# Performance work log

Measured on AMD Instinct MI355X. Metric: run time of the kernel, lower is better.

Reference implementation:

```python
import jax, jax.numpy as jnp
import numpy as np

B, S, D, H = 4, 2048, 1024, 16
DK = D // H
WINDOW = 256
GLOBAL = 16
NEG_INF = float(np.finfo(np.float32).min)


def local_window_mask(seq_len, window, global_tokens):
    # 0 where attention allowed, -inf where |i-j| > window and neither i nor j is a global token
    i = jnp.arange(seq_len)[:, None]
    j = jnp.arange(seq_len)[None, :]
    is_global = (i < global_tokens) | (j < global_tokens)
    out_of_window = jnp.abs(i - j) > window
    return jnp.where(out_of_window & ~is_global, NEG_INF, 0.0).astype(jnp.float32)


def setup_inputs() -> dict:
    key = jax.random.key(0)
    ks = jax.random.split(key, 8)
    std = 1.0 / np.sqrt(D)
    return {
        "q": jax.random.normal(ks[0], (B, S, D), jnp.float32),
        "k": jax.random.normal(ks[1], (B, S, D), jnp.float32),
        "v": jax.random.normal(ks[2], (B, S, D), jnp.float32),
        "attn_mask": jnp.zeros((B, S), jnp.float32),
        "wq": jax.random.normal(ks[3], (D, D), jnp.float32) * std,
        "bq": jnp.zeros((D,), jnp.float32),
        "wk": jax.random.normal(ks[4], (D, D), jnp.float32) * std,
        "bk": jnp.zeros((D,), jnp.float32),
        "wv": jax.random.normal(ks[5], (D, D), jnp.float32) * std,
        "bv": jnp.zeros((D,), jnp.float32),
        "wo": jax.random.normal(ks[6], (D, D), jnp.float32) * std,
        "bo": jnp.zeros((D,), jnp.float32),
    }


def reference(q, k, v, attn_mask, wq, bq, wk, bk, wv, bv, wo, bo):
    b, s, d = q.shape
    # projections (x @ W + b)
    Q = (q @ wq + bq).reshape(b, s, H, DK).transpose(0, 2, 1, 3)  # b h s dk
    K = (k @ wk + bk).reshape(b, s, H, DK).transpose(0, 2, 1, 3)
    V = (v @ wv + bv).reshape(b, s, H, DK).transpose(0, 2, 1, 3)

    scale = 1.0 / np.sqrt(DK)
    scores = jnp.einsum("bhqd,bhkd->bhqk", Q, K) * scale  # b h s s
    # additive key mask broadcast over query positions: attn_mask[:, None, None, :]
    scores = scores + attn_mask[:, None, None, :]
    scores = scores + local_window_mask(s, WINDOW, GLOBAL)[None, None, :, :]
    probs = jax.nn.softmax(scores, axis=-1)
    out = jnp.einsum("bhqk,bhkd->bhqd", probs, V)  # b h s dk
    out = out.transpose(0, 2, 1, 3).reshape(b, s, d)
    return out @ wo + bo
```

## Files before the change

### kernel.cpp

```cpp
#include <hip/hip_runtime.h>


#define B_   4
#define S_   2048
#define D_   1024
#define H_   16
#define DK_  64
#define WIN_ 256
#define GLB_ 16

typedef __attribute__((ext_vector_type(8))) short bf16x8;
typedef __attribute__((ext_vector_type(4))) float floatx4;

__device__ __forceinline__ unsigned short f2bf(float x) {
  unsigned u = __float_as_uint(x);
  unsigned r = u + 0x7FFFu + ((u >> 16) & 1u);
  return (unsigned short)(r >> 16);
}
__device__ __forceinline__ float bf2f(unsigned short h) {
  return __uint_as_float(((unsigned)h) << 16);
}
__device__ __forceinline__ void gload_lds16(const void* g, void* l) {
  __builtin_amdgcn_global_load_lds(
      (const __attribute__((address_space(1))) unsigned int*)g,
      (__attribute__((address_space(3))) unsigned int*)l, 16, 0, 0);
}

__global__ void split_bf16(const float* __restrict__ x,
                           unsigned short* __restrict__ hi,
                           unsigned short* __restrict__ lo)
{
  const int i = blockIdx.x * 256 + threadIdx.x;
  const float4 v = ((const float4*)x)[i];
  unsigned short h0 = f2bf(v.x), h1 = f2bf(v.y), h2 = f2bf(v.z), h3 = f2bf(v.w);
  unsigned short l0 = f2bf(v.x - bf2f(h0)), l1 = f2bf(v.y - bf2f(h1));
  unsigned short l2 = f2bf(v.z - bf2f(h2)), l3 = f2bf(v.w - bf2f(h3));
  unsigned long long hp = (unsigned long long)h0 | ((unsigned long long)h1 << 16)
                        | ((unsigned long long)h2 << 32) | ((unsigned long long)h3 << 48);
  unsigned long long lp = (unsigned long long)l0 | ((unsigned long long)l1 << 16)
                        | ((unsigned long long)l2 << 32) | ((unsigned long long)l3 << 48);
  ((unsigned long long*)hi)[i] = hp;
  ((unsigned long long*)lo)[i] = lp;
}

__global__ void wtsplit(const float* __restrict__ W,
                        unsigned short* __restrict__ hiT,
                        unsigned short* __restrict__ loT)
{
  __shared__ float t[32][33];
  const int bx = blockIdx.x * 32;
  const int by = blockIdx.y * 32;
  const int c = threadIdx.x & 31;
  const int r0 = (threadIdx.x >> 5) * 4;
#pragma unroll
  for (int i = 0; i < 4; ++i)
    t[r0 + i][c] = W[(size_t)(by + r0 + i) * 1024 + bx + c];
  __syncthreads();
#pragma unroll
  for (int i = 0; i < 4; ++i) {
    const int r = r0 + i;
    const float val = t[c][r];
    const unsigned short h = f2bf(val);
    hiT[(size_t)(bx + r) * 1024 + by + c] = h;
    loT[(size_t)(bx + r) * 1024 + by + c] = f2bf(val - bf2f(h));
  }
}

__global__ __launch_bounds__(256, 2) void gemm_mfma(
    const unsigned short* __restrict__ Ahi, const unsigned short* __restrict__ Alo,
    const unsigned short* __restrict__ WThi, const unsigned short* __restrict__ WTlo,
    const float* __restrict__ bias, float* __restrict__ Cf,
    unsigned short* __restrict__ Chi, unsigned short* __restrict__ Clo, int mode)
{
  __shared__ unsigned short AsH[4096], AsL[4096], WsH[4096], WsL[4096];
  const int tid = threadIdx.x;
  const int w = tid >> 6, lane = tid & 63;
  const int wr = w >> 1, wc = w & 1;
  const int bm = blockIdx.y * 128, bn = blockIdx.x * 128;
  const int lrow = lane & 15, lk8 = (lane >> 4) * 8;

  floatx4 acc[4][4];
#pragma unroll
  for (int t = 0; t < 4; ++t)
#pragma unroll
    for (int u = 0; u < 4; ++u) acc[t][u] = (floatx4){0.f, 0.f, 0.f, 0.f};

  const unsigned short* gsrc;
  unsigned short* lbase;
  int growbase;
  if      (w == 0) { gsrc = Ahi;  lbase = AsH; growbase = bm; }
  else if (w == 1) { gsrc = Alo;  lbase = AsL; growbase = bm; }
  else if (w == 2) { gsrc = WThi; lbase = WsH; growbase = bn; }
  else             { gsrc = WTlo; lbase = WsL; growbase = bn; }

  for (int k0 = 0; k0 < 1024; k0 += 32) {
    __syncthreads();
#pragma unroll
    for (int g = 0; g < 8; ++g) {
      const unsigned short* gp =
          gsrc + (size_t)(growbase + g * 16 + lrow) * 1024 + k0 + lk8;
      gload_lds16(gp, lbase + g * 512);
    }
    __syncthreads();

    bf16x8 ah[4], al[4], bh[4], bl[4];
#pragma unroll
    for (int t = 0; t < 4; ++t) {
      ah[t] = *(const bf16x8*)&AsH[(wr * 4 + t) * 512 + lane * 8];
      al[t] = *(const bf16x8*)&AsL[(wr * 4 + t) * 512 + lane * 8];
    }
#pragma unroll
    for (int u = 0; u < 4; ++u) {
      bh[u] = *(const bf16x8*)&WsH[(wc * 4 + u) * 512 + lane * 8];
      bl[u] = *(const bf16x8*)&WsL[(wc * 4 + u) * 512 + lane * 8];
    }
#pragma unroll
    for (int t = 0; t < 4; ++t)
#pragma unroll
      for (int u = 0; u < 4; ++u) {
        acc[t][u] = __builtin_amdgcn_mfma_f32_16x16x32_bf16(al[t], bh[u], acc[t][u], 0, 0, 0);
        acc[t][u] = __builtin_amdgcn_mfma_f32_16x16x32_bf16(ah[t], bl[u], acc[t][u], 0, 0, 0);
        acc[t][u] = __builtin_amdgcn_mfma_f32_16x16x32_bf16(ah[t], bh[u], acc[t][u], 0, 0, 0);
      }
  }

  float bs[4];
#pragma unroll
  for (int u = 0; u < 4; ++u) bs[u] = bias[bn + wc * 64 + u * 16 + lrow];

#pragma unroll
  for (int t = 0; t < 4; ++t)
#pragma unroll
    for (int r = 0; r < 4; ++r) {
      const int row = bm + wr * 64 + t * 16 + (lane >> 4) * 4 + r;
#pragma unroll
      for (int u = 0; u < 4; ++u) {
        const int col = bn + wc * 64 + u * 16 + lrow;
        const float val = acc[t][u][r] + bs[u];
        if (mode == 0) {
          Cf[(size_t)row * 1024 + col] = val;
        } else {
          const int bb = row >> 11, s = row & 2047;
          const int hh = col >> 6, dk = col & 63;
          if (mode == 1) {
            const size_t a = ((size_t)(bb * H_ + hh) * S_ + s) * DK_ + dk;
            const unsigned short hv = f2bf(val);
            Chi[a] = hv;
            Clo[a] = f2bf(val - bf2f(hv));
          } else {
            Chi[((size_t)(bb * H_ + hh) * DK_ + dk) * S_ + s] = f2bf(val);
          }
        }
      }
    }
}

__global__ __launch_bounds__(256, 4) void attn_mfma(
    const unsigned short* __restrict__ Qhi, const unsigned short* __restrict__ Qlo,
    const unsigned short* __restrict__ Khi, const unsigned short* __restrict__ Klo,
    const unsigned short* __restrict__ Vt,  const float* __restrict__ amask,
    unsigned short* __restrict__ AOhi, unsigned short* __restrict__ AOlo)
{
  __shared__ unsigned short lds[16384];

  const int tid = threadIdx.x;
  const int w = tid >> 6, lane = tid & 63;
  const int quad = lane >> 4, lm = lane & 15;
  const int qt = blockIdx.x, h = blockIdx.y, b = blockIdx.z;
  const int i0 = qt * 64;

  const size_t hb = (size_t)(b * H_ + h) * S_ * DK_;
  const unsigned short* Qhih = Qhi + hb;
  const unsigned short* Qloh = Qlo + hb;
  const unsigned short* Khih = Khi + hb;
  const unsigned short* Kloh = Klo + hb;
  const unsigned short* Vth  = Vt  + hb;

  bf16x8 aqh[2], aql[2];
#pragma unroll
  for (int p = 0; p < 2; ++p) {
    const size_t qa = (size_t)(i0 + w * 16 + lm) * DK_ + p * 32 + quad * 8;
    aqh[p] = *(const bf16x8*)(Qhih + qa);
    aql[p] = *(const bf16x8*)(Qloh + qa);
  }

  floatx4 acc_o[4];
  float m_i[4], l_i[4];
#pragma unroll
  for (int u = 0; u < 4; ++u) acc_o[u] = (floatx4){0.f, 0.f, 0.f, 0.f};
#pragma unroll
  for (int r = 0; r < 4; ++r) { m_i[r] = -1e30f; l_i[r] = 0.f; }

  int start, t_lo, t_hi;
  if (qt == 0) { start = 0; t_lo = 0; t_hi = 31; }
  else {
    start = -1;
    t_lo = qt - 4 < 1 ? 1 : qt - 4;
    t_hi = qt + 4 > 31 ? 31 : qt + 4;
  }

  unsigned short* Pb = &lds[12288 + w * 1024];

  for (int tt = start; tt <= t_hi; ++tt) {
    if (tt >= 0 && tt < t_lo) continue;
    const int kt = (tt < 0) ? 0 : tt;
    const int k0 = kt * 64;

    __syncthreads();
    for (int e = w; e < 24; e += 4) {
      const int op = e >> 3, cc = e & 7, g = cc >> 1, hf = cc & 1;
      unsigned short* ldst = &lds[op * 4096 + g * 1024 + hf * 512];
      const unsigned short* gp;
      if (op == 0)      gp = Khih + (size_t)(k0 + g * 16 + lm) * DK_ + (hf * 4 + quad) * 8;
      else if (op == 1) gp = Kloh + (size_t)(k0 + g * 16 + lm) * DK_ + (hf * 4 + quad) * 8;
      else              gp = Vth + (size_t)(g * 16 + lm) * S_ + k0 + (hf * 4 + quad) * 8;
      gload_lds16(gp, ldst);
    }
    __syncthreads();

    floatx4 sc[4];
#pragma unroll
    for (int u = 0; u < 4; ++u) sc[u] = (floatx4){0.f, 0.f, 0.f, 0.f};
#pragma unroll
    for (int u = 0; u < 4; ++u)
#pragma unroll
      for (int p = 0; p < 2; ++p) {
        const bf16x8 kh = *(const bf16x8*)&lds[       u * 1024 + p * 512 + lane * 8];
        const bf16x8 kl = *(const bf16x8*)&lds[4096 + u * 1024 + p * 512 + lane * 8];
        sc[u] = __builtin_amdgcn_mfma_f32_16x16x32_bf16(aql[p], kh, sc[u], 0, 0, 0);
        sc[u] = __builtin_amdgcn_mfma_f32_16x16x32_bf16(aqh[p], kl, sc[u], 0, 0, 0);
        sc[u] = __builtin_amdgcn_mfma_f32_16x16x32_bf16(aqh[p], kh, sc[u], 0, 0, 0);
      }

    float am4[4];
#pragma unroll
    for (int u = 0; u < 4; ++u) am4[u] = amask[b * S_ + k0 + u * 16 + lm];

    const int ibase = i0 + w * 16 + quad * 4;
#pragma unroll
    for (int r = 0; r < 4; ++r) {
      const int i = ibase + r;
      float mx = -1e30f;
#pragma unroll
      for (int u = 0; u < 4; ++u) {
        const int j = k0 + u * 16 + lm;
        const int diff = i - j;
        const bool ok = (diff <= WIN_ && diff >= -WIN_) || (i < GLB_) || (j < GLB_);
        const float sv = ok ? fmaf(sc[u][r], 0.125f, am4[u]) : -1e30f;
        sc[u][r] = sv;
        mx = fmaxf(mx, sv);
      }
#pragma unroll
      for (int st = 1; st <= 8; st <<= 1) mx = fmaxf(mx, __shfl_xor(mx, st));
      const float mn = fmaxf(m_i[r], mx);
      const float alpha = __expf(m_i[r] - mn);
      m_i[r] = mn;
      float rsum = 0.f;
#pragma unroll
      for (int u = 0; u < 4; ++u) {
        const float pv = __expf(sc[u][r] - mn);
        sc[u][r] = pv;
        rsum += pv;
      }
#pragma unroll
      for (int st = 1; st <= 8; st <<= 1) rsum += __shfl_xor(rsum, st);
      l_i[r] = l_i[r] * alpha + rsum;
#pragma unroll
      for (int u = 0; u < 4; ++u) acc_o[u][r] *= alpha;
    }

#pragma unroll
    for (int u = 0; u < 4; ++u) {
      const int key = u * 16 + lm;
      const int cbase = (key >> 3) * 128 + (key & 7);
#pragma unroll
      for (int r = 0; r < 4; ++r)
        Pb[cbase + (quad * 4 + r) * 8] = f2bf(sc[u][r]);
    }

#pragma unroll
    for (int p = 0; p < 2; ++p) {
      const bf16x8 pf = *(const bf16x8*)&Pb[p * 512 + lane * 8];
#pragma unroll
      for (int u = 0; u < 4; ++u) {
        const bf16x8 vf = *(const bf16x8*)&lds[8192 + u * 1024 + p * 512 + lane * 8];
        acc_o[u] = __builtin_amdgcn_mfma_f32_16x16x32_bf16(pf, vf, acc_o[u], 0, 0, 0);
      }
    }
  }

#pragma unroll
  for (int r = 0; r < 4; ++r) {
    const float linv = 1.0f / l_i[r];
    const size_t rowa = (size_t)(b * S_ + i0 + w * 16 + quad * 4 + r) * D_;
#pragma unroll
    for (int u = 0; u < 4; ++u) {
      const float val = acc_o[u][r] * linv;
      const size_t a = rowa + h * DK_ + u * 16 + lm;
      const unsigned short hv = f2bf(val);
      AOhi[a] = hv;
      AOlo[a] = f2bf(val - bf2f(hv));
    }
  }
}

#define BM 128
#define BN 128
#define BK 16

__global__ __launch_bounds__(256, 2) void gemm_f32(
    const float* __restrict__ A, const float* __restrict__ W,
    const float* __restrict__ bias, float* __restrict__ C, int mode)
{
  __shared__ float As[BK][BM + 4];
  __shared__ float Bs[BK][BN + 4];
  const int tid = threadIdx.x;
  const int bm = blockIdx.y * BM;
  const int bn = blockIdx.x * BN;
  const int tx = tid & 15;
  const int ty = tid >> 4;
  const int K = 1024, N = 1024;

  float acc[8][8];
#pragma unroll
  for (int i = 0; i < 8; ++i)
#pragma unroll
    for (int j = 0; j < 8; ++j) acc[i][j] = 0.f;

  const int arow = tid >> 2;
  const int acol = (tid & 3) * 4;
  const int brow = tid >> 5;
  const int bcol = (tid & 31) * 4;

  for (int k0 = 0; k0 < K; k0 += BK) {
    float4 a0 = *(const float4*)(A + (size_t)(bm + arow) * K + k0 + acol);
    float4 a1 = *(const float4*)(A + (size_t)(bm + arow + 64) * K + k0 + acol);
    float4 b0 = *(const float4*)(W + (size_t)(k0 + brow) * N + bn + bcol);
    float4 b1 = *(const float4*)(W + (size_t)(k0 + brow + 8) * N + bn + bcol);
    __syncthreads();
    As[acol + 0][arow] = a0.x; As[acol + 1][arow] = a0.y;
    As[acol + 2][arow] = a0.z; As[acol + 3][arow] = a0.w;
    As[acol + 0][arow + 64] = a1.x; As[acol + 1][arow + 64] = a1.y;
    As[acol + 2][arow + 64] = a1.z; As[acol + 3][arow + 64] = a1.w;
    *(float4*)&Bs[brow][bcol]     = b0;
    *(float4*)&Bs[brow + 8][bcol] = b1;
    __syncthreads();
#pragma unroll
    for (int kk = 0; kk < BK; ++kk) {
      float a[8], bb[8];
      float4 t;
      t = *(float4*)&As[kk][ty * 8];     a[0]=t.x; a[1]=t.y; a[2]=t.z; a[3]=t.w;
      t = *(float4*)&As[kk][ty * 8 + 4]; a[4]=t.x; a[5]=t.y; a[6]=t.z; a[7]=t.w;
      t = *(float4*)&Bs[kk][tx * 8];     bb[0]=t.x; bb[1]=t.y; bb[2]=t.z; bb[3]=t.w;
      t = *(float4*)&Bs[kk][tx * 8 + 4]; bb[4]=t.x; bb[5]=t.y; bb[6]=t.z; bb[7]=t.w;
#pragma unroll
      for (int i = 0; i < 8; ++i)
#pragma unroll
        for (int j = 0; j < 8; ++j)
          acc[i][j] = fmaf(a[i], bb[j], acc[i][j]);
    }
  }

  const float4 bias0 = *(const float4*)(bias + bn + tx * 8);
  const float4 bias1 = *(const float4*)(bias + bn + tx * 8 + 4);
  if (mode == 0) {
#pragma unroll
    for (int i = 0; i < 8; ++i) {
      const int m = bm + ty * 8 + i;
      float* dst = C + (size_t)m * 1024 + bn + tx * 8;
      *(float4*)dst = make_float4(acc[i][0] + bias0.x, acc[i][1] + bias0.y,
                                  acc[i][2] + bias0.z, acc[i][3] + bias0.w);
      *(float4*)(dst + 4) = make_float4(acc[i][4] + bias1.x, acc[i][5] + bias1.y,
                                        acc[i][6] + bias1.z, acc[i][7] + bias1.w);
    }
  } else {
    const int ncol = bn + tx * 8;
    const int h  = ncol >> 6;
    const int dk = ncol & 63;
#pragma unroll
    for (int i = 0; i < 8; ++i) {
      const int m = bm + ty * 8 + i;
      const int bb2 = m >> 11;
      const int s  = m & 2047;
      float* dst = C + ((size_t)(bb2 * H_ + h) * S_ + s) * DK_ + dk;
      *(float4*)dst = make_float4(acc[i][0] + bias0.x, acc[i][1] + bias0.y,
                                  acc[i][2] + bias0.z, acc[i][3] + bias0.w);
      *(float4*)(dst + 4) = make_float4(acc[i][4] + bias1.x, acc[i][5] + bias1.y,
                                        acc[i][6] + bias1.z, acc[i][7] + bias1.w);
    }
  }
}

__global__ __launch_bounds__(256, 2) void attn_v3(
    const float* __restrict__ Qp, const float* __restrict__ Kp,
    const float* __restrict__ Vp, const float* __restrict__ amask,
    float* __restrict__ AO)
{
  __shared__ float Qs[64][68], Ks[64][68], Vs[64][68], Ps[64][68];

  const int tid = threadIdx.x;
  const int qt = blockIdx.x;
  const int h  = blockIdx.y;
  const int b  = blockIdx.z;
  const int i0 = qt * 64;
  const int tr = tid >> 4;
  const int tc = tid & 15;

  const size_t head_off = (size_t)(b * H_ + h) * S_ * DK_;
  const float* Qh = Qp + head_off;
  const float* Kh = Kp + head_off;
  const float* Vh = Vp + head_off;

#pragma unroll
  for (int r = 0; r < 4; ++r) {
    const int f = tid + r * 256;
    const int row = f >> 4, col = (f & 15) * 4;
    *(float4*)&Qs[row][col] = *(const float4*)(Qh + (size_t)(i0 + row) * DK_ + col);
  }

  float m_i[4], l_i[4];
  float4 acc[4];
#pragma unroll
  for (int i = 0; i < 4; ++i) {
    m_i[i] = -1e30f; l_i[i] = 0.f;
    acc[i] = make_float4(0.f, 0.f, 0.f, 0.f);
  }

  int start, t_lo, t_hi;
  if (qt == 0) { start = 0; t_lo = 0; t_hi = 31; }
  else {
    start = -1;
    t_lo = qt - 4 < 1 ? 1 : qt - 4;
    t_hi = qt + 4 > 31 ? 31 : qt + 4;
  }

  for (int tt = start; tt <= t_hi; ++tt) {
    if (tt >= 0 && tt < t_lo) continue;
    const int kt = (tt < 0) ? 0 : tt;
    const int k0 = kt * 64;

    __syncthreads();
#pragma unroll
    for (int r = 0; r < 4; ++r) {
      const int f = tid + r * 256;
      const int row = f >> 4, col = (f & 15) * 4;
      *(float4*)&Ks[row][col] = *(const float4*)(Kh + (size_t)(k0 + row) * DK_ + col);
      *(float4*)&Vs[row][col] = *(const float4*)(Vh + (size_t)(k0 + row) * DK_ + col);
    }
    __syncthreads();

    float am[4];
#pragma unroll
    for (int u = 0; u < 4; ++u) am[u] = amask[b * S_ + k0 + tc + 16 * u];

    float s[4][4];
#pragma unroll
    for (int i = 0; i < 4; ++i)
#pragma unroll
      for (int u = 0; u < 4; ++u) s[i][u] = 0.f;
#pragma unroll
    for (int d4 = 0; d4 < 16; ++d4) {
      const float4 k0v = *(float4*)&Ks[tc     ][d4 * 4];
      const float4 k1v = *(float4*)&Ks[tc + 16][d4 * 4];
      const float4 k2v = *(float4*)&Ks[tc + 32][d4 * 4];
      const float4 k3v = *(float4*)&Ks[tc + 48][d4 * 4];
#pragma unroll
      for (int i = 0; i < 4; ++i) {
        const float4 q = *(float4*)&Qs[tr * 4 + i][d4 * 4];
        s[i][0] += q.x*k0v.x + q.y*k0v.y + q.z*k0v.z + q.w*k0v.w;
        s[i][1] += q.x*k1v.x + q.y*k1v.y + q.z*k1v.z + q.w*k1v.w;
        s[i][2] += q.x*k2v.x + q.y*k2v.y + q.z*k2v.z + q.w*k2v.w;
        s[i][3] += q.x*k3v.x + q.y*k3v.y + q.z*k3v.z + q.w*k3v.w;
      }
    }

#pragma unroll
    for (int i = 0; i < 4; ++i) {
      const int irow = i0 + tr * 4 + i;
#pragma unroll
      for (int u = 0; u < 4; ++u) {
        const int j = k0 + tc + 16 * u;
        const int diff = irow - j;
        const bool allowed = (diff <= WIN_ && diff >= -WIN_) || (irow < GLB_) || (j < GLB_);
        s[i][u] = allowed ? fmaf(s[i][u], 0.125f, am[u]) : -1e30f;
      }
    }

    float mt[4];
#pragma unroll
    for (int i = 0; i < 4; ++i)
      mt[i] = fmaxf(fmaxf(s[i][0], s[i][1]), fmaxf(s[i][2], s[i][3]));
#pragma unroll
    for (int st = 1; st <= 8; st <<= 1)
#pragma unroll
      for (int i = 0; i < 4; ++i)
        mt[i] = fmaxf(mt[i], __shfl_xor(mt[i], st));

    float alpha[4], rs[4];
#pragma unroll
    for (int i = 0; i < 4; ++i) {
      const float mn = fmaxf(m_i[i], mt[i]);
      alpha[i] = __expf(m_i[i] - mn);
      m_i[i] = mn;
      float r = 0.f;
#pragma unroll
      for (int u = 0; u < 4; ++u) {
        s[i][u] = __expf(s[i][u] - mn);
        r += s[i][u];
      }
      rs[i] = r;
    }
#pragma unroll
    for (int st = 1; st <= 8; st <<= 1)
#pragma unroll
      for (int i = 0; i < 4; ++i)
        rs[i] += __shfl_xor(rs[i], st);
#pragma unroll
    for (int i = 0; i < 4; ++i) {
      l_i[i] = l_i[i] * alpha[i] + rs[i];
      acc[i].x *= alpha[i]; acc[i].y *= alpha[i];
      acc[i].z *= alpha[i]; acc[i].w *= alpha[i];
    }

#pragma unroll
    for (int u = 0; u < 4; ++u)
      *(float4*)&Ps[tc + 16 * u][tr * 4] =
          make_float4(s[0][u], s[1][u], s[2][u], s[3][u]);
    __syncthreads();

#pragma unroll 4
    for (int j = 0; j < 64; ++j) {
      const float4 p4 = *(float4*)&Ps[j][tr * 4];
      const float4 v4 = *(float4*)&Vs[j][tc * 4];
      acc[0].x = fmaf(p4.x, v4.x, acc[0].x); acc[0].y = fmaf(p4.x, v4.y, acc[0].y);
      acc[0].z = fmaf(p4.x, v4.z, acc[0].z); acc[0].w = fmaf(p4.x, v4.w, acc[0].w);
      acc[1].x = fmaf(p4.y, v4.x, acc[1].x); acc[1].y = fmaf(p4.y, v4.y, acc[1].y);
      acc[1].z = fmaf(p4.y, v4.z, acc[1].z); acc[1].w = fmaf(p4.y, v4.w, acc[1].w);
      acc[2].x = fmaf(p4.z, v4.x, acc[2].x); acc[2].y = fmaf(p4.z, v4.y, acc[2].y);
      acc[2].z = fmaf(p4.z, v4.z, acc[2].z); acc[2].w = fmaf(p4.z, v4.w, acc[2].w);
      acc[3].x = fmaf(p4.w, v4.x, acc[3].x); acc[3].y = fmaf(p4.w, v4.y, acc[3].y);
      acc[3].z = fmaf(p4.w, v4.z, acc[3].z); acc[3].w = fmaf(p4.w, v4.w, acc[3].w);
    }
  }

#pragma unroll
  for (int i = 0; i < 4; ++i) {
    const float linv = 1.0f / l_i[i];
    const int row = i0 + tr * 4 + i;
    float* dst = AO + ((size_t)b * S_ + row) * D_ + h * DK_ + tc * 4;
    *(float4*)dst = make_float4(acc[i].x * linv, acc[i].y * linv,
                                acc[i].z * linv, acc[i].w * linv);
  }
}

extern "C" void kernel_launch(void* const* d_in, const int* in_sizes, int n_in,
                              void* d_out, int out_size, void* d_ws, size_t ws_size,
                              hipStream_t stream) {
  const float* q  = (const float*)d_in[0];
  const float* k  = (const float*)d_in[1];
  const float* v  = (const float*)d_in[2];
  const float* am = (const float*)d_in[3];
  const float* wq = (const float*)d_in[4];
  const float* bq = (const float*)d_in[5];
  const float* wk = (const float*)d_in[6];
  const float* bk = (const float*)d_in[7];
  const float* wv = (const float*)d_in[8];
  const float* bv = (const float*)d_in[9];
  const float* wo = (const float*)d_in[10];
  const float* bo = (const float*)d_in[11];
  float* out = (float*)d_out;

  const size_t PER = (size_t)B_ * H_ * S_ * DK_;
  const size_t NEED = 138412032;

  if (ws_size >= NEED) {
    unsigned short* us = (unsigned short*)d_ws;
    unsigned short* ACTh = us;
    unsigned short* ACTl = us + PER;
    unsigned short* Qhi  = us + 2 * PER;
    unsigned short* Qlo  = us + 3 * PER;
    unsigned short* Khi  = us + 4 * PER;
    unsigned short* Klo  = us + 5 * PER;
    unsigned short* Vtp  = us + 6 * PER;
    unsigned short* WHI  = us + 7 * PER;
    unsigned short* WLO  = WHI + 1048576;

    const int sgrid = (int)(PER / 4 / 256);
    dim3 wgrid(32, 32);
    dim3 ggrid(8, 64);

    split_bf16<<<sgrid, 256, 0, stream>>>(q, ACTh, ACTl);
    wtsplit<<<wgrid, 256, 0, stream>>>(wq, WHI, WLO);
    gemm_mfma<<<ggrid, 256, 0, stream>>>(ACTh, ACTl, WHI, WLO, bq, nullptr, Qhi, Qlo, 1);

    split_bf16<<<sgrid, 256, 0, stream>>>(k, ACTh, ACTl);
    wtsplit<<<wgrid, 256, 0, stream>>>(wk, WHI, WLO);
    gemm_mfma<<<ggrid, 256, 0, stream>>>(ACTh, ACTl, WHI, WLO, bk, nullptr, Khi, Klo, 1);

    split_bf16<<<sgrid, 256, 0, stream>>>(v, ACTh, ACTl);
    wtsplit<<<wgrid, 256, 0, stream>>>(wv, WHI, WLO);
    gemm_mfma<<<ggrid, 256, 0, stream>>>(ACTh, ACTl, WHI, WLO, bv, nullptr, Vtp, nullptr, 2);

    attn_mfma<<<dim3(S_ / 64, H_, B_), 256, 0, stream>>>(
        Qhi, Qlo, Khi, Klo, Vtp, am, ACTh, ACTl);

    wtsplit<<<wgrid, 256, 0, stream>>>(wo, WHI, WLO);
    gemm_mfma<<<ggrid, 256, 0, stream>>>(ACTh, ACTl, WHI, WLO, bo, out, nullptr, nullptr, 0);
  } else {
    float* Qp = (float*)d_ws;
    float* Kp = Qp + PER;
    float* Vp = Kp + PER;
    float* AOf = Vp + PER;
    dim3 gg(D_ / BN, (B_ * S_) / BM);
    gemm_f32<<<gg, 256, 0, stream>>>(q, wq, bq, Qp, 1);
    gemm_f32<<<gg, 256, 0, stream>>>(k, wk, bk, Kp, 1);
    gemm_f32<<<gg, 256, 0, stream>>>(v, wv, bv, Vp, 1);
    attn_v3<<<dim3(S_ / 64, H_, B_), 256, 0, stream>>>(Qp, Kp, Vp, am, AOf);
    gemm_f32<<<gg, 256, 0, stream>>>(AOf, wo, bo, out, 0);
  }
}
```

Before: 749.7 us.

## Transpose attention MFMA operands so each lane owns one query row

Swaps the A/B operands of the QK^T and PV MFMAs so the accumulator holds scores transposed, giving each lane a single query row with 16 keys. Softmax max/sum reductions shrink from per-row 4-step shuffles across 16 lanes to two cross-quad shuffles with a single m/l state per lane. P is written to LDS as packed 64-bit stores, the mask is read as float4, and output stores become 64-bit packed writes instead of scalar 16-bit stores. This cuts shuffle and scalar store traffic, at the cost of a changed LDS write pattern that may introduce bank conflicts.

```diff
diff --git a/kernel.cpp b/kernel.cpp
--- a/kernel.cpp
+++ b/kernel.cpp
@@ -176,20 +176,20 @@
   const unsigned short* Kloh = Klo + hb;
   const unsigned short* Vth  = Vt  + hb;
 
-  bf16x8 aqh[2], aql[2];
+  const int myrow = i0 + w * 16 + lm;
+
+  bf16x8 bqh[2], bql[2];
 #pragma unroll
   for (int p = 0; p < 2; ++p) {
-    const size_t qa = (size_t)(i0 + w * 16 + lm) * DK_ + p * 32 + quad * 8;
-    aqh[p] = *(const bf16x8*)(Qhih + qa);
-    aql[p] = *(const bf16x8*)(Qloh + qa);
-  }
-
-  floatx4 acc_o[4];
-  float m_i[4], l_i[4];
-#pragma unroll
-  for (int u = 0; u < 4; ++u) acc_o[u] = (floatx4){0.f, 0.f, 0.f, 0.f};
-#pragma unroll
-  for (int r = 0; r < 4; ++r) { m_i[r] = -1e30f; l_i[r] = 0.f; }
+    const size_t qa = (size_t)myrow * DK_ + p * 32 + quad * 8;
+    bqh[p] = *(const bf16x8*)(Qhih + qa);
+    bql[p] = *(const bf16x8*)(Qloh + qa);
+  }
+
+  floatx4 acc[4];
+  float m_i = -1e30f, l_i = 0.f;
+#pragma unroll
+  for (int u = 0; u < 4; ++u) acc[u] = (floatx4){0.f, 0.f, 0.f, 0.f};
 
   int start, t_lo, t_hi;
   if (qt == 0) { start = 0; t_lo = 0; t_hi = 31; }
@@ -199,7 +199,8 @@
     t_hi = qt + 4 > 31 ? 31 : qt + 4;
   }
 
-  unsigned short* Pb = &lds[12288 + w * 1024];
+  unsigned short* Pw = &lds[12288 + w * 1024];
+  const bool iglb = (myrow < GLB_);
 
   for (int tt = start; tt <= t_hi; ++tt) {
     if (tt >= 0 && tt < t_lo) continue;
@@ -227,80 +228,87 @@
       for (int p = 0; p < 2; ++p) {
         const bf16x8 kh = *(const bf16x8*)&lds[       u * 1024 + p * 512 + lane * 8];
         const bf16x8 kl = *(const bf16x8*)&lds[4096 + u * 1024 + p * 512 + lane * 8];
-        sc[u] = __builtin_amdgcn_mfma_f32_16x16x32_bf16(aql[p], kh, sc[u], 0, 0, 0);
-        sc[u] = __builtin_amdgcn_mfma_f32_16x16x32_bf16(aqh[p], kl, sc[u], 0, 0, 0);
-        sc[u] = __builtin_amdgcn_mfma_f32_16x16x32_bf16(aqh[p], kh, sc[u], 0, 0, 0);
-      }
-
-    float am4[4];
-#pragma unroll
-    for (int u = 0; u < 4; ++u) am4[u] = amask[b * S_ + k0 + u * 16 + lm];
-
-    const int ibase = i0 + w * 16 + quad * 4;
-#pragma unroll
-    for (int r = 0; r < 4; ++r) {
-      const int i = ibase + r;
-      float mx = -1e30f;
-#pragma unroll
-      for (int u = 0; u < 4; ++u) {
-        const int j = k0 + u * 16 + lm;
-        const int diff = i - j;
-        const bool ok = (diff <= WIN_ && diff >= -WIN_) || (i < GLB_) || (j < GLB_);
-        const float sv = ok ? fmaf(sc[u][r], 0.125f, am4[u]) : -1e30f;
+        sc[u] = __builtin_amdgcn_mfma_f32_16x16x32_bf16(kh, bql[p], sc[u], 0, 0, 0);
+        sc[u] = __builtin_amdgcn_mfma_f32_16x16x32_bf16(kl, bqh[p], sc[u], 0, 0, 0);
+        sc[u] = __builtin_amdgcn_mfma_f32_16x16x32_bf16(kh, bqh[p], sc[u], 0, 0, 0);
+      }
+
+    float mx = -1e30f;
+#pragma unroll
+    for (int u = 0; u < 4; ++u) {
+      const float4 amv = *(const float4*)(amask + b * S_ + k0 + u * 16 + quad * 4);
+      const float amr[4] = {amv.x, amv.y, amv.z, amv.w};
+#pragma unroll
+      for (int r = 0; r < 4; ++r) {
+        const int j = k0 + u * 16 + quad * 4 + r;
+        const int diff = myrow - j;
+        const bool ok = (diff <= WIN_ && diff >= -WIN_) || iglb || (j < GLB_);
+        const float sv = ok ? fmaf(sc[u][r], 0.125f, amr[r]) : -1e30f;
         sc[u][r] = sv;
         mx = fmaxf(mx, sv);
       }
-#pragma unroll
-      for (int st = 1; st <= 8; st <<= 1) mx = fmaxf(mx, __shfl_xor(mx, st));
-      const float mn = fmaxf(m_i[r], mx);
-      const float alpha = __expf(m_i[r] - mn);
-      m_i[r] = mn;
-      float rsum = 0.f;
-#pragma unroll
-      for (int u = 0; u < 4; ++u) {
+    }
+    mx = fmaxf(mx, __shfl_xor(mx, 16));
+    mx = fmaxf(mx, __shfl_xor(mx, 32));
+
+    const float mn = fmaxf(m_i, mx);
+    const float alpha = __expf(m_i - mn);
+    m_i = mn;
+    float rsum = 0.f;
+#pragma unroll
+    for (int u = 0; u < 4; ++u)
+#pragma unroll
+      for (int r = 0; r < 4; ++r) {
         const float pv = __expf(sc[u][r] - mn);
         sc[u][r] = pv;
         rsum += pv;
       }
-#pragma unroll
-      for (int st = 1; st <= 8; st <<= 1) rsum += __shfl_xor(rsum, st);
-      l_i[r] = l_i[r] * alpha + rsum;
-#pragma unroll
-      for (int u = 0; u < 4; ++u) acc_o[u][r] *= alpha;
-    }
-
+    rsum += __shfl_xor(rsum, 16);
+    rsum += __shfl_xor(rsum, 32);
+    l_i = l_i * alpha + rsum;
 #pragma unroll
     for (int u = 0; u < 4; ++u) {
-      const int key = u * 16 + lm;
-      const int cbase = (key >> 3) * 128 + (key & 7);
-#pragma unroll
-      for (int r = 0; r < 4; ++r)
-        Pb[cbase + (quad * 4 + r) * 8] = f2bf(sc[u][r]);
+      acc[u][0] *= alpha; acc[u][1] *= alpha;
+      acc[u][2] *= alpha; acc[u][3] *= alpha;
+    }
+
+#pragma unroll
+    for (int u = 0; u < 4; ++u) {
+      const unsigned long long pk =
+          (unsigned long long)f2bf(sc[u][0])
+        | ((unsigned long long)f2bf(sc[u][1]) << 16)
+        | ((unsigned long long)f2bf(sc[u][2]) << 32)
+        | ((unsigned long long)f2bf(sc[u][3]) << 48);
+      *(unsigned long long*)&Pw[(u * 2 + (quad >> 1)) * 128 + lm * 8 + (quad & 1) * 4] = pk;
     }
 
 #pragma unroll
     for (int p = 0; p < 2; ++p) {
-      const bf16x8 pf = *(const bf16x8*)&Pb[p * 512 + lane * 8];
+      const bf16x8 pf = *(const bf16x8*)&Pw[p * 512 + lane * 8];
 #pragma unroll
       for (int u = 0; u < 4; ++u) {
         const bf16x8 vf = *(const bf16x8*)&lds[8192 + u * 1024 + p * 512 + lane * 8];
-        acc_o[u] = __builtin_amdgcn_mfma_f32_16x16x32_bf16(pf, vf, acc_o[u], 0, 0, 0);
-      }
-    }
-  }
-
-#pragma unroll
-  for (int r = 0; r < 4; ++r) {
-    const float linv = 1.0f / l_i[r];
-    const size_t rowa = (size_t)(b * S_ + i0 + w * 16 + quad * 4 + r) * D_;
-#pragma unroll
-    for (int u = 0; u < 4; ++u) {
-      const float val = acc_o[u][r] * linv;
-      const size_t a = rowa + h * DK_ + u * 16 + lm;
-      const unsigned short hv = f2bf(val);
-      AOhi[a] = hv;
-      AOlo[a] = f2bf(val - bf2f(hv));
-    }
+        acc[u] = __builtin_amdgcn_mfma_f32_16x16x32_bf16(vf, pf, acc[u], 0, 0, 0);
+      }
+    }
+  }
+
+  const float linv = 1.0f / l_i;
+  const size_t rowa = (size_t)(b * S_ + myrow) * D_ + h * DK_;
+#pragma unroll
+  for (int u = 0; u < 4; ++u) {
+    float vv[4];
+    unsigned short hv[4];
+#pragma unroll
+    for (int r = 0; r < 4; ++r) { vv[r] = acc[u][r] * linv; hv[r] = f2bf(vv[r]); }
+    unsigned long long hp = (unsigned long long)hv[0] | ((unsigned long long)hv[1] << 16)
+                          | ((unsigned long long)hv[2] << 32) | ((unsigned long long)hv[3] << 48);
+    unsigned long long lp = 0;
+#pragma unroll
+    for (int r = 0; r < 4; ++r)
+      lp |= ((unsigned long long)f2bf(vv[r] - bf2f(hv[r]))) << (16 * r);
+    *(unsigned long long*)&AOhi[rowa + u * 16 + quad * 4] = hp;
+    *(unsigned long long*)&AOlo[rowa + u * 16 + quad * 4] = lp;
   }
 }
 
```

Result: no change. 752.3 us (+0.4%).
